# Kernel optimization log

Hardware: AMD Instinct MI355X
Metric: run time of the kernel (lower is better)

## Reference

```python
import jax, jax.numpy as jnp
import numpy as np

B, S, H = 2, 2048, 2560
NH, NKV, D = 8, 4, 256
SW = 1024
EPS = 1e-6
NEG = -1e9


def _rms(x, w=None, eps=EPS):
    y = x * jax.lax.rsqrt(jnp.mean(x * x, axis=-1, keepdims=True) + eps)
    return y * (1.0 + w) if w is not None else y


def _rope(x, cos, sin):
    # x: [B, h, S, D]; cos/sin: [1, 1, S, D] with duplicated half-frequencies
    half = x.shape[-1] // 2
    out = x * cos
    o1 = out[..., :half] - x[..., half:] * sin[..., :half]
    o2 = out[..., half:] + x[..., :half] * sin[..., half:]
    return jnp.concatenate([o1, o2], axis=-1)


def setup_inputs() -> dict:
    key = jax.random.key(0)
    ks = jax.random.split(key, 6)
    hidden_states = jax.random.normal(ks[0], (B, S, H), dtype=jnp.float32)
    Wq = jax.random.normal(ks[1], (NH * D, H), dtype=jnp.float32) * 0.02
    Wk = jax.random.normal(ks[2], (NKV * D, H), dtype=jnp.float32) * 0.02
    Wv = jax.random.normal(ks[3], (NKV * D, H), dtype=jnp.float32) * 0.02
    Wo = jax.random.normal(ks[4], (H, NH * D), dtype=jnp.float32) * 0.02
    q_norm_w = jnp.zeros((D,), dtype=jnp.float32)
    k_norm_w = jnp.zeros((D,), dtype=jnp.float32)
    # RoPE tables (standard theta=10000, duplicated halves as in torch ref)
    pos = jnp.arange(S, dtype=jnp.float32)
    inv = 1.0 / (10000.0 ** (jnp.arange(0, D, 2, dtype=jnp.float32) / D))
    freqs = pos[:, None] * inv[None, :]            # [S, D/2]
    emb = jnp.concatenate([freqs, freqs], axis=-1)  # [S, D]
    cos = jnp.cos(emb)[None, None]                 # [1,1,S,D]
    sin = jnp.sin(emb)[None, None]
    # causal + sliding-window additive mask (allowed: i-SW < j <= i)
    i = jnp.arange(S)[:, None]
    j = jnp.arange(S)[None, :]
    allowed = (j <= i) & (j > i - SW)
    attention_mask = jnp.where(allowed, 0.0, NEG).astype(jnp.float32)[None, None]
    return {"hidden_states": hidden_states, "attention_mask": attention_mask,
            "cos": cos, "sin": sin, "Wq": Wq, "Wk": Wk, "Wv": Wv, "Wo": Wo,
            "q_norm_w": q_norm_w, "k_norm_w": k_norm_w}


def reference(hidden_states, attention_mask, cos, sin, Wq, Wk, Wv, Wo, q_norm_w, k_norm_w):
    b, s, _ = hidden_states.shape
    xq = (hidden_states @ Wq.T).reshape(b, s, NH, D).transpose(0, 2, 1, 3)  # [B,NH,S,D]
    xq = _rms(xq, q_norm_w)
    xk = (hidden_states @ Wk.T).reshape(b, s, NKV, D)
    xv = (hidden_states @ Wv.T).reshape(b, s, NKV, D)
    xk = _rms(xk, k_norm_w)
    xv = _rms(xv)  # parameterless rms_norm on v
    xk = xk.transpose(0, 2, 1, 3)  # [B,NKV,S,D]
    xv = xv.transpose(0, 2, 1, 3)
    xq = _rope(xq, cos, sin)
    xk = _rope(xk, cos, sin)
    # expand_kv path: S >= sliding_window and NH != NKV -> repeat_interleave
    g = NH // NKV
    xk = jnp.repeat(xk, g, axis=1)
    xv = jnp.repeat(xv, g, axis=1)
    # scale=1.0 in original (no 1/sqrt(d))
    scores = jnp.einsum('bhqd,bhkd->bhqk', xq, xk) + attention_mask
    attn = jax.nn.softmax(scores, axis=-1)
    out = jnp.einsum('bhqk,bhkd->bhqd', attn, xv)
    out = out.transpose(0, 2, 1, 3).reshape(b, s, NH * D)
    return out @ Wo.T
```

## Files before the change

kernel.cpp:

```cpp
#include <hip/hip_runtime.h>

#define B_   2
#define S_   2048
#define H_   2560
#define NH_  8
#define NKV_ 4
#define D_   256
#define SW_  1024

#define QKV_LD 4096

typedef __attribute__((ext_vector_type(8))) short    short8;
typedef __attribute__((ext_vector_type(8))) _Float16 half8;
typedef __attribute__((ext_vector_type(4))) _Float16 half4;
typedef __attribute__((ext_vector_type(4))) float    floatx4;
typedef __attribute__((ext_vector_type(2))) float    floatx2;

typedef unsigned int __attribute__((address_space(1))) as1_uint;
typedef unsigned int __attribute__((address_space(3))) as3_uint;

static __device__ __forceinline__ void async16(const void* g, void* l) {
    __builtin_amdgcn_global_load_lds((const as1_uint*)g, (as3_uint*)l, 16, 0, 0);
}

__global__ __launch_bounds__(256) void conv_f32_f16(
    const float* __restrict__ src, _Float16* __restrict__ dst, int n4)
{
    for (int i = blockIdx.x * 256 + threadIdx.x; i < n4; i += gridDim.x * 256) {
        floatx4 v = *(const floatx4*)(src + (size_t)i * 4);
        half4 h = { (_Float16)v.x, (_Float16)v.y, (_Float16)v.z, (_Float16)v.w };
        *(half4*)(dst + (size_t)i * 4) = h;
    }
}

template <int C_FP32>
__global__ __launch_bounds__(256, 2) void gemm_f16(
    const _Float16* __restrict__ A,
    const _Float16* __restrict__ Bm,
    void* __restrict__ Cv,
    int M, int N, int K)
{
    __shared__ __align__(16) _Float16 As[128 * 32];
    __shared__ __align__(16) _Float16 Bs[128 * 32];

    const int tid  = threadIdx.x;
    const int lane = tid & 63, w = tid >> 6;
    const int wr = w >> 1, wc = w & 1;
    const int quad = lane >> 4, l16 = lane & 15;
    const int mBase = blockIdx.y * 128, nBase = blockIdx.x * 128;

    floatx4 acc[4][4];
    const floatx4 fzero = {0.f, 0.f, 0.f, 0.f};
#pragma unroll
    for (int i = 0; i < 4; ++i)
#pragma unroll
        for (int j = 0; j < 4; ++j) acc[i][j] = fzero;

    const int sRow = lane >> 2;
    const int sCol = (lane & 3) * 8;
    const size_t aRow = (size_t)(mBase + w * 32 + sRow);
    const size_t bRow = (size_t)(nBase + w * 32 + sRow);

    for (int kk = 0; kk < K; kk += 32) {
#pragma unroll
        for (int i = 0; i < 2; ++i) {
            async16(A  + (aRow + i * 16) * K + kk + sCol, &As[(w * 32 + i * 16) * 32]);
            async16(Bm + (bRow + i * 16) * K + kk + sCol, &Bs[(w * 32 + i * 16) * 32]);
        }
        __syncthreads();
        half8 af[4], bfv[4];
#pragma unroll
        for (int i = 0; i < 4; ++i)
            af[i] = *(const half8*)&As[(wr * 64 + i * 16 + l16) * 32 + quad * 8];
#pragma unroll
        for (int j = 0; j < 4; ++j)
            bfv[j] = *(const half8*)&Bs[(wc * 64 + j * 16 + l16) * 32 + quad * 8];
#pragma unroll
        for (int i = 0; i < 4; ++i)
#pragma unroll
            for (int j = 0; j < 4; ++j)
                acc[i][j] = __builtin_amdgcn_mfma_f32_16x16x32_f16(af[i], bfv[j], acc[i][j], 0, 0, 0);
        __syncthreads();
    }

#pragma unroll
    for (int i = 0; i < 4; ++i) {
        const int row0 = mBase + wr * 64 + i * 16 + quad * 4;
#pragma unroll
        for (int j = 0; j < 4; ++j) {
            const int col = nBase + wc * 64 + j * 16 + l16;
#pragma unroll
            for (int r = 0; r < 4; ++r) {
                const size_t idx = (size_t)(row0 + r) * N + col;
                if (C_FP32) ((float*)Cv)[idx] = acc[i][j][r];
                else        ((_Float16*)Cv)[idx] = (_Float16)acc[i][j][r];
            }
        }
    }
}

__global__ __launch_bounds__(256) void rmsrope_inplace(
    _Float16* __restrict__ qkv,
    const float* __restrict__ cosT,
    const float* __restrict__ sinT,
    const float* __restrict__ qw,
    const float* __restrict__ kw)
{
    const int t = blockIdx.x;
    const int s = t & (S_ - 1);
    const int tid = threadIdx.x, lane = tid & 63, w = tid >> 6;
    _Float16* row = qkv + (size_t)t * QKV_LD;
    const int d0 = lane * 2, d1 = 128 + lane * 2;

    floatx2 c0 = *(const floatx2*)(cosT + (size_t)s * D_ + d0);
    floatx2 c1 = *(const floatx2*)(cosT + (size_t)s * D_ + d1);
    floatx2 s0 = *(const floatx2*)(sinT + (size_t)s * D_ + d0);
    floatx2 s1 = *(const floatx2*)(sinT + (size_t)s * D_ + d1);
    floatx2 qw0 = *(const floatx2*)(qw + d0), qw1 = *(const floatx2*)(qw + d1);
    floatx2 kw0 = *(const floatx2*)(kw + d0), kw1 = *(const floatx2*)(kw + d1);

#pragma unroll
    for (int p = 0; p < 4; ++p) {
        const int v = w + p * 4;
        _Float16* x = row + v * D_;
        float x0a = (float)x[d0], x0b = (float)x[d0 + 1];
        float x1a = (float)x[d1], x1b = (float)x[d1 + 1];
        float ss = x0a * x0a + x0b * x0b + x1a * x1a + x1b * x1b;
#pragma unroll
        for (int off = 32; off > 0; off >>= 1) ss += __shfl_xor(ss, off, 64);
        const float rinv = rsqrtf(ss * (1.0f / 256.0f) + 1e-6f);
        if (v < 8) {
            const float y0a = x0a * rinv * (1.f + qw0.x), y0b = x0b * rinv * (1.f + qw0.y);
            const float y1a = x1a * rinv * (1.f + qw1.x), y1b = x1b * rinv * (1.f + qw1.y);
            x[d0] = (_Float16)(y0a * c0.x - y1a * s0.x);
            x[d0 + 1] = (_Float16)(y0b * c0.y - y1b * s0.y);
            x[d1] = (_Float16)(y1a * c1.x + y0a * s1.x);
            x[d1 + 1] = (_Float16)(y1b * c1.y + y0b * s1.y);
        } else if (v < 12) {
            const float y0a = x0a * rinv * (1.f + kw0.x), y0b = x0b * rinv * (1.f + kw0.y);
            const float y1a = x1a * rinv * (1.f + kw1.x), y1b = x1b * rinv * (1.f + kw1.y);
            x[d0] = (_Float16)(y0a * c0.x - y1a * s0.x);
            x[d0 + 1] = (_Float16)(y0b * c0.y - y1b * s0.y);
            x[d1] = (_Float16)(y1a * c1.x + y0a * s1.x);
            x[d1 + 1] = (_Float16)(y1b * c1.y + y0b * s1.y);
        } else {
            x[d0] = (_Float16)(x0a * rinv);
            x[d0 + 1] = (_Float16)(x0b * rinv);
            x[d1] = (_Float16)(x1a * rinv);
            x[d1 + 1] = (_Float16)(x1b * rinv);
        }
    }
}

#define KS_STRIDE 264
#define VS_STRIDE 40
#define PS_STRIDE 40

__global__ __launch_bounds__(256, 2) void attn_kernel(
    const _Float16* __restrict__ qkv,
    _Float16* __restrict__ Oa)
{
    __shared__ __align__(16) _Float16 Ks[32 * KS_STRIDE];
    __shared__ __align__(16) _Float16 Vs[256 * VS_STRIDE];
    __shared__ __align__(16) _Float16 Ps[4][16 * PS_STRIDE];

    const int qb = blockIdx.x * 64;
    const int h = blockIdx.y, b = blockIdx.z;
    const int kvh = h >> 1;
    const int tid = threadIdx.x, lane = tid & 63, w = tid >> 6;
    const int quad = lane >> 4, l16 = lane & 15;

    const _Float16* Qrow = qkv + ((size_t)(b * S_ + qb + w * 16 + l16)) * QKV_LD + h * D_;
    half8 qf[8];
#pragma unroll
    for (int kst = 0; kst < 8; ++kst)
        qf[kst] = *(const half8*)(Qrow + kst * 32 + quad * 8);

    floatx4 o[16];
    const floatx4 fzero = {0.f, 0.f, 0.f, 0.f};
#pragma unroll
    for (int dt = 0; dt < 16; ++dt) o[dt] = fzero;
    float mrow[4] = {-1e30f, -1e30f, -1e30f, -1e30f};
    float lrow[4] = {0.f, 0.f, 0.f, 0.f};

    const _Float16* Kbase = qkv + (size_t)(b * S_) * QKV_LD + 2048 + kvh * D_;
    const _Float16* Vbase = qkv + (size_t)(b * S_) * QKV_LD + 3072 + kvh * D_;
    const int kb_start = (qb >= SW_) ? qb - SW_ : 0;
    const int kb_end = qb + 32;

    for (int kb = kb_start; kb <= kb_end; kb += 32) {
#pragma unroll
        for (int p = 0; p < 4; ++p) {
            const int c = tid + p * 256;
            const int r = c >> 5, off = (c & 31) * 8;
            *(half8*)&Ks[r * KS_STRIDE + off] = *(const half8*)(Kbase + (size_t)(kb + r) * QKV_LD + off);
        }
#pragma unroll
        for (int p = 0; p < 4; ++p) {
            const int c = tid + p * 256;
            const int r = c & 31, vd0 = (c >> 5) * 8;
            half8 vv = *(const half8*)(Vbase + (size_t)(kb + r) * QKV_LD + vd0);
#pragma unroll
            for (int j = 0; j < 8; ++j)
                Vs[(vd0 + j) * VS_STRIDE + r] = vv[j];
        }
        __syncthreads();

        floatx4 sacc[2];
        sacc[0] = fzero; sacc[1] = fzero;
#pragma unroll
        for (int jt = 0; jt < 2; ++jt)
#pragma unroll
            for (int kst = 0; kst < 8; ++kst) {
                half8 kf = *(const half8*)&Ks[(jt * 16 + l16) * KS_STRIDE + kst * 32 + quad * 8];
                sacc[jt] = __builtin_amdgcn_mfma_f32_16x16x32_f16(qf[kst], kf, sacc[jt], 0, 0, 0);
            }

        const int q0 = qb + w * 16 + quad * 4;
        float sval[2][4], tmax[4];
#pragma unroll
        for (int r = 0; r < 4; ++r) tmax[r] = -1e30f;
#pragma unroll
        for (int jt = 0; jt < 2; ++jt) {
            const int kg = kb + jt * 16 + l16;
#pragma unroll
            for (int r = 0; r < 4; ++r) {
                const int qg = q0 + r;
                const bool ok = (kg <= qg) && (kg + SW_ > qg);
                const float vv = ok ? sacc[jt][r] : -1e30f;
                sval[jt][r] = vv;
                tmax[r] = fmaxf(tmax[r], vv);
            }
        }
#pragma unroll
        for (int r = 0; r < 4; ++r) {
#pragma unroll
            for (int off = 1; off < 16; off <<= 1)
                tmax[r] = fmaxf(tmax[r], __shfl_xor(tmax[r], off, 64));
            const float mnew = fmaxf(mrow[r], tmax[r]);
            const float alpha = __expf(mrow[r] - mnew);
            mrow[r] = mnew;
            lrow[r] *= alpha;
            tmax[r] = alpha;
        }
        float rsum[4] = {0.f, 0.f, 0.f, 0.f};
#pragma unroll
        for (int jt = 0; jt < 2; ++jt)
#pragma unroll
            for (int r = 0; r < 4; ++r) {
                float pv = __expf(sval[jt][r] - mrow[r]);
                pv = (sval[jt][r] <= -1e29f) ? 0.0f : pv;
                rsum[r] += pv;
                Ps[w][(quad * 4 + r) * PS_STRIDE + jt * 16 + l16] = (_Float16)pv;
            }
#pragma unroll
        for (int r = 0; r < 4; ++r) {
#pragma unroll
            for (int off = 1; off < 16; off <<= 1)
                rsum[r] += __shfl_xor(rsum[r], off, 64);
            lrow[r] += rsum[r];
        }
#pragma unroll
        for (int dt = 0; dt < 16; ++dt)
#pragma unroll
            for (int r = 0; r < 4; ++r) o[dt][r] *= tmax[r];

        half8 pa = *(const half8*)&Ps[w][l16 * PS_STRIDE + quad * 8];
#pragma unroll
        for (int dt = 0; dt < 16; ++dt) {
            half8 vf = *(const half8*)&Vs[(dt * 16 + l16) * VS_STRIDE + quad * 8];
            o[dt] = __builtin_amdgcn_mfma_f32_16x16x32_f16(pa, vf, o[dt], 0, 0, 0);
        }
        __syncthreads();
    }

    const int qrow = qb + w * 16 + quad * 4;
#pragma unroll
    for (int r = 0; r < 4; ++r) {
        const float inv = (lrow[r] > 0.f) ? (1.0f / lrow[r]) : 0.f;
        _Float16* orow = Oa + ((size_t)(b * S_ + qrow + r)) * (NH_ * D_) + h * D_;
#pragma unroll
        for (int dt = 0; dt < 16; ++dt)
            orow[dt * 16 + l16] = (_Float16)(o[dt][r] * inv);
    }
}

extern "C" void kernel_launch(void* const* d_in, const int* in_sizes, int n_in,
                              void* d_out, int out_size, void* d_ws, size_t ws_size,
                              hipStream_t stream)
{
    (void)in_sizes; (void)n_in; (void)out_size; (void)ws_size;
    const float* hid  = (const float*)d_in[0];
    const float* cosT = (const float*)d_in[2];
    const float* sinT = (const float*)d_in[3];
    const float* Wq   = (const float*)d_in[4];
    const float* Wk   = (const float*)d_in[5];
    const float* Wv   = (const float*)d_in[6];
    const float* Wo   = (const float*)d_in[7];
    const float* qw   = (const float*)d_in[8];
    const float* kw   = (const float*)d_in[9];
    float* out = (float*)d_out;

    char* ws = (char*)d_ws;
    _Float16* qkv  = (_Float16*)(ws);
    _Float16* attn = (_Float16*)(ws + 33554432ull);
    _Float16* hidH = (_Float16*)(ws + 50331648ull);
    _Float16* wQKV = (_Float16*)(ws + 71303168ull);
    _Float16* woH  = (_Float16*)(ws + 92274688ull);

    const int nHid = 4096 * 2560 / 4;
    const int nWq  = 2048 * 2560 / 4;
    const int nWkv = 1024 * 2560 / 4;
    const int nWo  = 2560 * 2048 / 4;

    conv_f32_f16<<<2048, 256, 0, stream>>>(hid, hidH, nHid);
    conv_f32_f16<<<1024, 256, 0, stream>>>(Wq, wQKV, nWq);
    conv_f32_f16<<<512,  256, 0, stream>>>(Wk, wQKV + (size_t)2048 * 2560, nWkv);
    conv_f32_f16<<<512,  256, 0, stream>>>(Wv, wQKV + (size_t)3072 * 2560, nWkv);
    conv_f32_f16<<<1024, 256, 0, stream>>>(Wo, woH, nWo);

    gemm_f16<0><<<dim3(32, 32), 256, 0, stream>>>(hidH, wQKV, qkv, 4096, 4096, 2560);
    rmsrope_inplace<<<4096, 256, 0, stream>>>(qkv, cosT, sinT, qw, kw);
    attn_kernel<<<dim3(32, 8, 2), 256, 0, stream>>>(qkv, attn);
    gemm_f16<1><<<dim3(20, 32), 256, 0, stream>>>(attn, woH, out, 4096, 2560, 2048);
}
```

Before: 453.2 us.

## Load K/V fragments directly from global, pre-transpose V, merge conversion launches

The five fp32-to-fp16 conversion launches are merged into one 2D-grid kernel. A new kernel transposes V into a [b,kvh,D,S] buffer. The attention kernel drops its shared-memory K/V staging and the two block barriers per tile, and loads K and V MFMA fragments straight from global memory into registers. This removes LDS traffic and barriers, but adds a transpose pass, repeated global reads of K/V by the four waves, and higher register pressure.

```diff
diff --git a/kernel.cpp b/kernel.cpp
--- a/kernel.cpp
+++ b/kernel.cpp
@@ -23,9 +23,22 @@
     __builtin_amdgcn_global_load_lds((const as1_uint*)g, (as3_uint*)l, 16, 0, 0);
 }
 
-__global__ __launch_bounds__(256) void conv_f32_f16(
-    const float* __restrict__ src, _Float16* __restrict__ dst, int n4)
-{
+__global__ __launch_bounds__(256) void conv_all(
+    const float* __restrict__ s0, const float* __restrict__ s1,
+    const float* __restrict__ s2, const float* __restrict__ s3,
+    const float* __restrict__ s4,
+    _Float16* __restrict__ d0, _Float16* __restrict__ d1,
+    _Float16* __restrict__ d2, _Float16* __restrict__ d3,
+    _Float16* __restrict__ d4)
+{
+    const float* src; _Float16* dst; int n4;
+    switch (blockIdx.y) {
+        case 0:  src = s0; dst = d0; n4 = 4096 * 2560 / 4; break;
+        case 1:  src = s1; dst = d1; n4 = 2048 * 2560 / 4; break;
+        case 2:  src = s2; dst = d2; n4 = 1024 * 2560 / 4; break;
+        case 3:  src = s3; dst = d3; n4 = 1024 * 2560 / 4; break;
+        default: src = s4; dst = d4; n4 = 2560 * 2048 / 4; break;
+    }
     for (int i = blockIdx.x * 256 + threadIdx.x; i < n4; i += gridDim.x * 256) {
         floatx4 v = *(const floatx4*)(src + (size_t)i * 4);
         half4 h = { (_Float16)v.x, (_Float16)v.y, (_Float16)v.z, (_Float16)v.w };
@@ -152,16 +165,31 @@
     }
 }
 
-#define KS_STRIDE 264
-#define VS_STRIDE 40
+__global__ __launch_bounds__(256) void transpose_v(
+    const _Float16* __restrict__ qkv, _Float16* __restrict__ Vt)
+{
+    __shared__ _Float16 tile[64][66];
+    const int s0 = blockIdx.x * 64;
+    const int dd0 = blockIdx.y * 64;
+    const int bk = blockIdx.z;
+    const int b = bk >> 2, kvh = bk & 3;
+    const _Float16* src = qkv + (size_t)(b * S_) * QKV_LD + 3072 + kvh * D_;
+    _Float16* dst = Vt + (size_t)bk * D_ * S_;
+    const int tx = threadIdx.x & 63, ty = threadIdx.x >> 6;
+    for (int r = ty; r < 64; r += 4)
+        tile[r][tx] = src[(size_t)(s0 + r) * QKV_LD + dd0 + tx];
+    __syncthreads();
+    for (int r = ty; r < 64; r += 4)
+        dst[(size_t)(dd0 + r) * S_ + s0 + tx] = tile[tx][r];
+}
+
 #define PS_STRIDE 40
 
 __global__ __launch_bounds__(256, 2) void attn_kernel(
     const _Float16* __restrict__ qkv,
+    const _Float16* __restrict__ Vt,
     _Float16* __restrict__ Oa)
 {
-    __shared__ __align__(16) _Float16 Ks[32 * KS_STRIDE];
-    __shared__ __align__(16) _Float16 Vs[256 * VS_STRIDE];
     __shared__ __align__(16) _Float16 Ps[4][16 * PS_STRIDE];
 
     const int qb = blockIdx.x * 64;
@@ -183,38 +211,27 @@
     float mrow[4] = {-1e30f, -1e30f, -1e30f, -1e30f};
     float lrow[4] = {0.f, 0.f, 0.f, 0.f};
 
-    const _Float16* Kbase = qkv + (size_t)(b * S_) * QKV_LD + 2048 + kvh * D_;
-    const _Float16* Vbase = qkv + (size_t)(b * S_) * QKV_LD + 3072 + kvh * D_;
+    const _Float16* Kbase  = qkv + (size_t)(b * S_) * QKV_LD + 2048 + kvh * D_;
+    const _Float16* Vtbase = Vt + (size_t)(b * NKV_ + kvh) * D_ * S_;
     const int kb_start = (qb >= SW_) ? qb - SW_ : 0;
     const int kb_end = qb + 32;
 
     for (int kb = kb_start; kb <= kb_end; kb += 32) {
-#pragma unroll
-        for (int p = 0; p < 4; ++p) {
-            const int c = tid + p * 256;
-            const int r = c >> 5, off = (c & 31) * 8;
-            *(half8*)&Ks[r * KS_STRIDE + off] = *(const half8*)(Kbase + (size_t)(kb + r) * QKV_LD + off);
-        }
-#pragma unroll
-        for (int p = 0; p < 4; ++p) {
-            const int c = tid + p * 256;
-            const int r = c & 31, vd0 = (c >> 5) * 8;
-            half8 vv = *(const half8*)(Vbase + (size_t)(kb + r) * QKV_LD + vd0);
-#pragma unroll
-            for (int j = 0; j < 8; ++j)
-                Vs[(vd0 + j) * VS_STRIDE + r] = vv[j];
-        }
-        __syncthreads();
-
+        half8 kf[2][8];
+#pragma unroll
+        for (int jt = 0; jt < 2; ++jt) {
+            const _Float16* kr = Kbase + (size_t)(kb + jt * 16 + l16) * QKV_LD + quad * 8;
+#pragma unroll
+            for (int kst = 0; kst < 8; ++kst)
+                kf[jt][kst] = *(const half8*)(kr + kst * 32);
+        }
         floatx4 sacc[2];
         sacc[0] = fzero; sacc[1] = fzero;
 #pragma unroll
         for (int jt = 0; jt < 2; ++jt)
 #pragma unroll
-            for (int kst = 0; kst < 8; ++kst) {
-                half8 kf = *(const half8*)&Ks[(jt * 16 + l16) * KS_STRIDE + kst * 32 + quad * 8];
-                sacc[jt] = __builtin_amdgcn_mfma_f32_16x16x32_f16(qf[kst], kf, sacc[jt], 0, 0, 0);
-            }
+            for (int kst = 0; kst < 8; ++kst)
+                sacc[jt] = __builtin_amdgcn_mfma_f32_16x16x32_f16(qf[kst], kf[jt][kst], sacc[jt], 0, 0, 0);
 
         const int q0 = qb + w * 16 + quad * 4;
         float sval[2][4], tmax[4];
@@ -266,12 +283,13 @@
             for (int r = 0; r < 4; ++r) o[dt][r] *= tmax[r];
 
         half8 pa = *(const half8*)&Ps[w][l16 * PS_STRIDE + quad * 8];
-#pragma unroll
-        for (int dt = 0; dt < 16; ++dt) {
-            half8 vf = *(const half8*)&Vs[(dt * 16 + l16) * VS_STRIDE + quad * 8];
-            o[dt] = __builtin_amdgcn_mfma_f32_16x16x32_f16(pa, vf, o[dt], 0, 0, 0);
-        }
-        __syncthreads();
+        half8 vf[16];
+#pragma unroll
+        for (int dt = 0; dt < 16; ++dt)
+            vf[dt] = *(const half8*)(Vtbase + (size_t)(dt * 16 + l16) * S_ + kb + quad * 8);
+#pragma unroll
+        for (int dt = 0; dt < 16; ++dt)
+            o[dt] = __builtin_amdgcn_mfma_f32_16x16x32_f16(pa, vf[dt], o[dt], 0, 0, 0);
     }
 
     const int qrow = qb + w * 16 + quad * 4;
@@ -307,20 +325,15 @@
     _Float16* hidH = (_Float16*)(ws + 50331648ull);
     _Float16* wQKV = (_Float16*)(ws + 71303168ull);
     _Float16* woH  = (_Float16*)(ws + 92274688ull);
-
-    const int nHid = 4096 * 2560 / 4;
-    const int nWq  = 2048 * 2560 / 4;
-    const int nWkv = 1024 * 2560 / 4;
-    const int nWo  = 2560 * 2048 / 4;
-
-    conv_f32_f16<<<2048, 256, 0, stream>>>(hid, hidH, nHid);
-    conv_f32_f16<<<1024, 256, 0, stream>>>(Wq, wQKV, nWq);
-    conv_f32_f16<<<512,  256, 0, stream>>>(Wk, wQKV + (size_t)2048 * 2560, nWkv);
-    conv_f32_f16<<<512,  256, 0, stream>>>(Wv, wQKV + (size_t)3072 * 2560, nWkv);
-    conv_f32_f16<<<1024, 256, 0, stream>>>(Wo, woH, nWo);
+    _Float16* Vt   = (_Float16*)(ws + 102760448ull);
+
+    conv_all<<<dim3(512, 5), 256, 0, stream>>>(
+        hid, Wq, Wk, Wv, Wo,
+        hidH, wQKV, wQKV + (size_t)2048 * 2560, wQKV + (size_t)3072 * 2560, woH);
 
     gemm_f16<0><<<dim3(32, 32), 256, 0, stream>>>(hidH, wQKV, qkv, 4096, 4096, 2560);
     rmsrope_inplace<<<4096, 256, 0, stream>>>(qkv, cosT, sinT, qw, kw);
-    attn_kernel<<<dim3(32, 8, 2), 256, 0, stream>>>(qkv, attn);
+    transpose_v<<<dim3(32, 4, 8), 256, 0, stream>>>(qkv, Vt);
+    attn_kernel<<<dim3(32, 8, 2), 256, 0, stream>>>(qkv, Vt, attn);
     gemm_f16<1><<<dim3(20, 32), 256, 0, stream>>>(attn, woH, out, 4096, 2560, 2048);
 }
```

New measurement: 590.9 us. +30.4%, slower.
